# Kernel tuning notes

Measured on AMD Instinct MI355X. Metric: run time of the kernel, lower is better.

The kernel has to match this reference:

```python
import jax, jax.numpy as jnp
import numpy as np

BETA = 0.25


def setup_inputs() -> dict:
    key = jax.random.key(0)
    k1, k2 = jax.random.split(key)
    latents = jax.random.normal(k1, (16, 4096, 256), dtype=jnp.float32)
    K = 1024
    # torch init: uniform(-1/K, 1/K)
    codebook = jax.random.uniform(k2, (K, 256), dtype=jnp.float32, minval=-1.0 / K, maxval=1.0 / K)
    return {"latents": latents, "codebook": codebook}


def reference(latents, codebook):
    D = codebook.shape[1]
    flat = latents.reshape(-1, D)  # [N, D]
    dist = (jnp.sum(flat * flat, axis=1, keepdims=True)
            + jnp.sum(codebook * codebook, axis=1)
            - 2.0 * jnp.matmul(flat, codebook.T))
    encoding_inds = jnp.argmin(dist, axis=1)  # [N]
    # gather nearest codebook vectors (equivalent to one-hot @ codebook)
    quantized = codebook[encoding_inds].reshape(latents.shape)
    commitment_loss = jnp.mean((jax.lax.stop_gradient(quantized) - latents) ** 2)
    embedding_loss = jnp.mean((quantized - jax.lax.stop_gradient(latents)) ** 2)
    vq_loss = commitment_loss * BETA + embedding_loss
    # straight-through estimator
    quantized_st = latents + jax.lax.stop_gradient(quantized - latents)
    return quantized_st, vq_loss
```

## Files before the change

kernel.cpp:

```cpp
#include <hip/hip_runtime.h>

typedef __attribute__((ext_vector_type(4))) float f32x4;
typedef __attribute__((ext_vector_type(2))) long i64x2;

#define SCALE 262144.0f
#define NEG2S -524288.0f
#define INV_S2 1.4551915228366852e-11f

static __device__ __forceinline__ unsigned umin2(unsigned a, unsigned b) { return a < b ? a : b; }

static __device__ __forceinline__ float dec_e4m3(unsigned b) {
  int e = (b >> 3) & 15, m = b & 7;
  float v = e ? ldexpf((float)(8 + m), e - 10) : ldexpf((float)m, -9);
  return (b & 0x80) ? -v : v;
}

__global__ void vq_prep(const float* __restrict__ cb,
                        float* __restrict__ norms,
                        unsigned char* __restrict__ cbh,
                        float* __restrict__ loss_out) {
  if (blockIdx.x == 0 && threadIdx.x == 0) *loss_out = 0.0f;
  const int lane = threadIdx.x & 63;
  const int code = (blockIdx.x * blockDim.x + threadIdx.x) >> 6;
  const f32x4 v = ((const f32x4*)(cb + (long)code * 256))[lane];
  unsigned w = __builtin_amdgcn_cvt_pk_fp8_f32(v[0] * SCALE, v[1] * SCALE, 0, false);
  w = __builtin_amdgcn_cvt_pk_fp8_f32(v[2] * SCALE, v[3] * SCALE, w, true);
  float n = 0.f;
#pragma unroll
  for (int j = 0; j < 4; ++j) {
    float d = dec_e4m3((w >> (8 * j)) & 0xFFu);
    n = __builtin_fmaf(d, d, n);
  }
  const int newpos = ((lane >> 1) & 3) * 64 + (lane >> 3) * 8 + (lane & 1) * 4;
  *(unsigned*)(cbh + (long)code * 256 + newpos) = w;
#pragma unroll
  for (int m = 1; m < 64; m <<= 1) n += __shfl_xor(n, m);
  if (lane == 0) norms[code] = n;
}

#define BM 128
#define DD 256
#define NTHR 512
#define CT 64
#define NSUB 16

__global__ __launch_bounds__(NTHR, 4)
void vq_main(const float* __restrict__ X,
             const float* __restrict__ CB,
             const float* __restrict__ norms_g,
             const unsigned char* __restrict__ cbh,
             float* __restrict__ out,
             float* __restrict__ loss_out,
             float lscale) {
  __shared__ __attribute__((aligned(16))) unsigned char Eb[2 * CT * DD];
  __shared__ __attribute__((aligned(16))) float nrmLds[1024];
  __shared__ float wsumX[8];
  __shared__ float wsumS[8];

  const int t = threadIdx.x;
  const int lane = t & 63;
  const int wave = t >> 6;
  const int lo16 = lane & 15;
  const int hi = lane >> 4;
  const long rowBase = (long)blockIdx.x * BM;

  const char* cbB = (const char*)cbh;
  char* ebBase = (char*)Eb;
#define STAGE_E(ST, BUF)                                                                      \
  {                                                                                           \
    _Pragma("unroll") for (int c = 0; c < 2; ++c) {                                           \
      unsigned o = (unsigned)(wave * 2048 + c * 1024 + lane * 16);                            \
      unsigned src = o ^ ((((o >> 8) & 7u)) << 4);                                            \
      __builtin_amdgcn_global_load_lds(                                                       \
          (const __attribute__((address_space(1))) void*)(cbB + (unsigned)(ST)*16384u + src), \
          (__attribute__((address_space(3))) void*)(ebBase + (BUF)*16384 + wave * 2048 + c * 1024), \
          16, 0, 0);                                                                          \
    }                                                                                         \
  }

  STAGE_E(0, 0);

  nrmLds[t] = norms_g[t];
  nrmLds[t + 512] = norms_g[t + 512];

  float xn = 0.f;
  long a[8];
  {
    const f32x4* xr = (const f32x4*)(X + (rowBase + wave * 16 + lo16) * DD);
#pragma unroll
    for (int ks = 0; ks < 8; ++ks) {
      f32x4 v0 = __builtin_nontemporal_load(xr + ks * 8 + hi * 2);
      f32x4 v1 = __builtin_nontemporal_load(xr + ks * 8 + hi * 2 + 1);
#pragma unroll
      for (int j = 0; j < 4; ++j) xn = __builtin_fmaf(v0[j], v0[j], xn);
#pragma unroll
      for (int j = 0; j < 4; ++j) xn = __builtin_fmaf(v1[j], v1[j], xn);
      unsigned w0 = __builtin_amdgcn_cvt_pk_fp8_f32(v0[0], v0[1], 0, false);
      w0 = __builtin_amdgcn_cvt_pk_fp8_f32(v0[2], v0[3], w0, true);
      unsigned w1 = __builtin_amdgcn_cvt_pk_fp8_f32(v1[0], v1[1], 0, false);
      w1 = __builtin_amdgcn_cvt_pk_fp8_f32(v1[2], v1[3], w1, true);
      a[ks] = (long)w0 | ((long)w1 << 32);
    }
  }
  __syncthreads();

  unsigned best[4];
#pragma unroll
  for (int r = 0; r < 4; ++r) best[r] = 0xFFFFFFFFu;

  const unsigned swzl = (unsigned)((lo16 & 7) << 4);
  unsigned nbase[4];
#pragma unroll
  for (int n = 0; n < 4; ++n) nbase[n] = (unsigned)((n * 16 + lo16) * 256) ^ swzl;
  const unsigned hi64 = (unsigned)(hi * 64);

#pragma unroll 2
  for (int st = 0; st < NSUB; ++st) {
    if (st + 1 < NSUB) {
      STAGE_E(st + 1, (st + 1) & 1);
      asm volatile("s_waitcnt vmcnt(2)" ::: "memory");
    } else {
      asm volatile("s_waitcnt vmcnt(0)" ::: "memory");
    }
    __builtin_amdgcn_s_barrier();
    __builtin_amdgcn_sched_barrier(0);

    const char* eb = ebBase + (st & 1) * 16384;
    f32x4 acc[4];
#pragma unroll
    for (int n = 0; n < 4; ++n) {
      f32x4 z = {0.f, 0.f, 0.f, 0.f};
      acc[n] = z;
    }
    __builtin_amdgcn_s_setprio(1);
#pragma unroll
    for (int kp = 0; kp < 4; ++kp) {
      const unsigned koff = hi64 + (unsigned)(kp * 16);
      i64x2 b0 = *(const i64x2*)(eb + (nbase[0] ^ koff));
      i64x2 b1 = *(const i64x2*)(eb + (nbase[1] ^ koff));
      i64x2 b2 = *(const i64x2*)(eb + (nbase[2] ^ koff));
      i64x2 b3 = *(const i64x2*)(eb + (nbase[3] ^ koff));
      acc[0] = __builtin_amdgcn_mfma_f32_16x16x32_fp8_fp8(a[2 * kp], b0.x, acc[0], 0, 0, 0);
      acc[1] = __builtin_amdgcn_mfma_f32_16x16x32_fp8_fp8(a[2 * kp], b1.x, acc[1], 0, 0, 0);
      acc[2] = __builtin_amdgcn_mfma_f32_16x16x32_fp8_fp8(a[2 * kp], b2.x, acc[2], 0, 0, 0);
      acc[3] = __builtin_amdgcn_mfma_f32_16x16x32_fp8_fp8(a[2 * kp], b3.x, acc[3], 0, 0, 0);
      acc[0] = __builtin_amdgcn_mfma_f32_16x16x32_fp8_fp8(a[2 * kp + 1], b0.y, acc[0], 0, 0, 0);
      acc[1] = __builtin_amdgcn_mfma_f32_16x16x32_fp8_fp8(a[2 * kp + 1], b1.y, acc[1], 0, 0, 0);
      acc[2] = __builtin_amdgcn_mfma_f32_16x16x32_fp8_fp8(a[2 * kp + 1], b2.y, acc[2], 0, 0, 0);
      acc[3] = __builtin_amdgcn_mfma_f32_16x16x32_fp8_fp8(a[2 * kp + 1], b3.y, acc[3], 0, 0, 0);
    }
    __builtin_amdgcn_s_setprio(0);

#pragma unroll
    for (int n = 0; n < 4; ++n) {
      float nf = nrmLds[st * 64 + n * 16 + lo16];
      unsigned code = (unsigned)(st * 64 + n * 16 + lo16);
#pragma unroll
      for (int r = 0; r < 4; ++r) {
        float sv = __builtin_fmaf(NEG2S, acc[n][r], nf);
        unsigned u = __float_as_uint(sv);
        u = ((int)u < 0) ? ~u : (u | 0x80000000u);
        best[r] = umin2(best[r], (u & 0xFFFFFC00u) | code);
      }
    }

    __builtin_amdgcn_sched_barrier(0);
    __builtin_amdgcn_s_barrier();
  }

#pragma unroll
  for (int r = 0; r < 4; ++r) {
#pragma unroll
    for (int msk = 1; msk < 16; msk <<= 1)
      best[r] = umin2(best[r], (unsigned)__shfl_xor((int)best[r], msk));
  }

#pragma unroll
  for (int msk = 1; msk < 64; msk <<= 1) xn += __shfl_xor(xn, msk);
  if (lane == 0) wsumX[wave] = xn;

  __syncthreads();
  unsigned* mg = (unsigned*)Eb;
  unsigned* idxArr = mg + BM;
  if (lo16 == 0) {
#pragma unroll
    for (int r = 0; r < 4; ++r) {
      mg[wave * 16 + hi * 4 + r] = best[r];
    }
  }
  __syncthreads();
  float sc = 0.f;
  if (t < BM) {
    unsigned e = mg[t];
    idxArr[t] = e & 1023u;
    unsigned um = (e & 0xFFFFFC00u) | 512u;
    float sr = (um & 0x80000000u) ? __uint_as_float(um & 0x7FFFFFFFu) : __uint_as_float(~um);
    sc = sr * INV_S2;
  }
#pragma unroll
  for (int msk = 1; msk < 64; msk <<= 1) sc += __shfl_xor(sc, msk);
  if (lane == 0) wsumS[wave] = sc;
  __syncthreads();

  {
    const f32x4* CBv = (const f32x4*)CB;
    f32x4* Og = (f32x4*)(out + rowBase * DD);
#pragma unroll 4
    for (int i = 0; i < 16; ++i) {
      int idx = t + NTHR * i;
      int row = idx >> 6, d4 = idx & 63;
      int code = (int)idxArr[row];
      f32x4 e = CBv[code * 64 + d4];
      __builtin_nontemporal_store(e, Og + idx);
    }
  }

  if (t == 0) {
    float tot = 0.f;
#pragma unroll
    for (int w = 0; w < 8; ++w) tot += wsumX[w] + wsumS[w];
    atomicAdd(loss_out, tot * lscale);
  }
}

extern "C" void kernel_launch(void* const* d_in, const int* in_sizes, int n_in,
                              void* d_out, int out_size, void* d_ws, size_t ws_size,
                              hipStream_t stream) {
  const float* X = (const float*)d_in[0];
  const float* CB = (const float*)d_in[1];
  float* out = (float*)d_out;

  const int ND = in_sizes[0];
  const int K = in_sizes[1] / DD;
  const int N = ND / DD;

  float* ws_norms = (float*)d_ws;
  unsigned char* ws_cb = (unsigned char*)((char*)d_ws + 4096);
  float* loss_out = out + (size_t)ND;

  vq_prep<<<K / 4, 256, 0, stream>>>(CB, ws_norms, ws_cb, loss_out);

  const float lscale = 1.25f / (float)ND;
  vq_main<<<N / BM, NTHR, 0, stream>>>(X, CB, ws_norms, ws_cb, out, loss_out, lscale);
}
```

Before: 56.95 us.

## Keep codebook slice resident in registers and stream latent tiles through LDS

Swaps the dataflow so each wave keeps its 128-code fp8 codebook slice and norms in registers for the whole block. 16-row latent tiles are converted to fp8 and double-buffered in LDS, and each wave writes its own per-tile argmin candidates for a final cross-wave min. Blocks now cover 256 rows instead of 128, and occupancy is lowered to 2 blocks per SIMD set to hold 64 extra registers of B fragments. This removes repeated streaming of the whole codebook through LDS per block. The cost is heavier register pressure, a barrier per tile, and fewer blocks in the grid.

Result: slower. 62.70 us (+10.1%).

```diff
diff --git a/kernel.cpp b/kernel.cpp
--- a/kernel.cpp
+++ b/kernel.cpp
@@ -38,13 +38,11 @@
   if (lane == 0) norms[code] = n;
 }
 
-#define BM 128
-#define DD 256
 #define NTHR 512
-#define CT 64
-#define NSUB 16
-
-__global__ __launch_bounds__(NTHR, 4)
+#define RPB 256
+#define NTILE 16
+
+__global__ __launch_bounds__(NTHR, 2)
 void vq_main(const float* __restrict__ X,
              const float* __restrict__ CB,
              const float* __restrict__ norms_g,
@@ -52,161 +50,146 @@
              float* __restrict__ out,
              float* __restrict__ loss_out,
              float lscale) {
-  __shared__ __attribute__((aligned(16))) unsigned char Eb[2 * CT * DD];
-  __shared__ __attribute__((aligned(16))) float nrmLds[1024];
-  __shared__ float wsumX[8];
-  __shared__ float wsumS[8];
+  __shared__ __attribute__((aligned(16))) unsigned char Xs[2][4096];
+  __shared__ unsigned mgAll[NTILE][8][16];
+  __shared__ unsigned idxArr[RPB];
+  __shared__ float wsumX[8], wsumS[8];
 
   const int t = threadIdx.x;
   const int lane = t & 63;
   const int wave = t >> 6;
   const int lo16 = lane & 15;
   const int hi = lane >> 4;
-  const long rowBase = (long)blockIdx.x * BM;
-
-  const char* cbB = (const char*)cbh;
-  char* ebBase = (char*)Eb;
-#define STAGE_E(ST, BUF)                                                                      \
-  {                                                                                           \
-    _Pragma("unroll") for (int c = 0; c < 2; ++c) {                                           \
-      unsigned o = (unsigned)(wave * 2048 + c * 1024 + lane * 16);                            \
-      unsigned src = o ^ ((((o >> 8) & 7u)) << 4);                                            \
-      __builtin_amdgcn_global_load_lds(                                                       \
-          (const __attribute__((address_space(1))) void*)(cbB + (unsigned)(ST)*16384u + src), \
-          (__attribute__((address_space(3))) void*)(ebBase + (BUF)*16384 + wave * 2048 + c * 1024), \
-          16, 0, 0);                                                                          \
-    }                                                                                         \
-  }
-
-  STAGE_E(0, 0);
-
-  nrmLds[t] = norms_g[t];
-  nrmLds[t + 512] = norms_g[t + 512];
+  const long rowBase = (long)blockIdx.x * RPB;
+
+  long b[8][8];
+  float nrm[8];
+  {
+    const char* cbB = (const char*)cbh;
+#pragma unroll
+    for (int n = 0; n < 8; ++n) {
+      const int code = wave * 128 + n * 16 + lo16;
+      const char* src = cbB + (long)code * 256 + hi * 64;
+#pragma unroll
+      for (int kp = 0; kp < 4; ++kp) {
+        i64x2 bb = *(const i64x2*)(src + kp * 16);
+        b[n][2 * kp] = bb.x;
+        b[n][2 * kp + 1] = bb.y;
+      }
+      nrm[n] = norms_g[code];
+    }
+  }
+
+  const int srow = t >> 5;
+  const int sch = t & 31;
+  const unsigned sdst =
+      (unsigned)(srow * 256 + ((((sch & 3) * 64) + ((sch >> 2) * 8)) ^ ((srow & 7) << 3)));
+  const f32x4* xv = (const f32x4*)(X + (rowBase + srow) * 256) + sch * 2;
 
   float xn = 0.f;
-  long a[8];
-  {
-    const f32x4* xr = (const f32x4*)(X + (rowBase + wave * 16 + lo16) * DD);
-#pragma unroll
-    for (int ks = 0; ks < 8; ++ks) {
-      f32x4 v0 = __builtin_nontemporal_load(xr + ks * 8 + hi * 2);
-      f32x4 v1 = __builtin_nontemporal_load(xr + ks * 8 + hi * 2 + 1);
-#pragma unroll
-      for (int j = 0; j < 4; ++j) xn = __builtin_fmaf(v0[j], v0[j], xn);
-#pragma unroll
-      for (int j = 0; j < 4; ++j) xn = __builtin_fmaf(v1[j], v1[j], xn);
-      unsigned w0 = __builtin_amdgcn_cvt_pk_fp8_f32(v0[0], v0[1], 0, false);
-      w0 = __builtin_amdgcn_cvt_pk_fp8_f32(v0[2], v0[3], w0, true);
-      unsigned w1 = __builtin_amdgcn_cvt_pk_fp8_f32(v1[0], v1[1], 0, false);
-      w1 = __builtin_amdgcn_cvt_pk_fp8_f32(v1[2], v1[3], w1, true);
-      a[ks] = (long)w0 | ((long)w1 << 32);
-    }
-  }
+  f32x4 p0, p1;
+
+#define CVT_WRITE(BUF)                                                                    \
+  {                                                                                       \
+    float s0 = 0.f;                                                                       \
+    _Pragma("unroll") for (int j = 0; j < 4; ++j) s0 = __builtin_fmaf(p0[j], p0[j], s0);  \
+    _Pragma("unroll") for (int j = 0; j < 4; ++j) s0 = __builtin_fmaf(p1[j], p1[j], s0);  \
+    xn += s0;                                                                             \
+    unsigned w0 = __builtin_amdgcn_cvt_pk_fp8_f32(p0[0], p0[1], 0, false);                \
+    w0 = __builtin_amdgcn_cvt_pk_fp8_f32(p0[2], p0[3], w0, true);                         \
+    unsigned w1 = __builtin_amdgcn_cvt_pk_fp8_f32(p1[0], p1[1], 0, false);                \
+    w1 = __builtin_amdgcn_cvt_pk_fp8_f32(p1[2], p1[3], w1, true);                         \
+    *(long*)((char*)&Xs[BUF][0] + sdst) = (long)(unsigned)w0 | ((long)w1 << 32);          \
+  }
+
+  p0 = __builtin_nontemporal_load(xv);
+  p1 = __builtin_nontemporal_load(xv + 1);
+  CVT_WRITE(0);
+  p0 = __builtin_nontemporal_load(xv + 1024);
+  p1 = __builtin_nontemporal_load(xv + 1024 + 1);
   __syncthreads();
 
-  unsigned best[4];
-#pragma unroll
-  for (int r = 0; r < 4; ++r) best[r] = 0xFFFFFFFFu;
-
-  const unsigned swzl = (unsigned)((lo16 & 7) << 4);
-  unsigned nbase[4];
-#pragma unroll
-  for (int n = 0; n < 4; ++n) nbase[n] = (unsigned)((n * 16 + lo16) * 256) ^ swzl;
-  const unsigned hi64 = (unsigned)(hi * 64);
-
-#pragma unroll 2
-  for (int st = 0; st < NSUB; ++st) {
-    if (st + 1 < NSUB) {
-      STAGE_E(st + 1, (st + 1) & 1);
-      asm volatile("s_waitcnt vmcnt(2)" ::: "memory");
-    } else {
-      asm volatile("s_waitcnt vmcnt(0)" ::: "memory");
-    }
-    __builtin_amdgcn_s_barrier();
-    __builtin_amdgcn_sched_barrier(0);
-
-    const char* eb = ebBase + (st & 1) * 16384;
-    f32x4 acc[4];
-#pragma unroll
-    for (int n = 0; n < 4; ++n) {
+  for (int tt = 0; tt < NTILE; ++tt) {
+    const char* xb = (const char*)&Xs[tt & 1][0];
+    const unsigned abase = (unsigned)(lo16 * 256 + hi * 64);
+    const unsigned aswz = (unsigned)((lo16 & 7) << 3);
+    long a[8];
+#pragma unroll
+    for (int ks = 0; ks < 8; ++ks)
+      a[ks] = *(const long*)(xb + ((abase + ks * 8) ^ aswz));
+
+    f32x4 acc[8];
+#pragma unroll
+    for (int n = 0; n < 8; ++n) {
       f32x4 z = {0.f, 0.f, 0.f, 0.f};
       acc[n] = z;
     }
     __builtin_amdgcn_s_setprio(1);
 #pragma unroll
-    for (int kp = 0; kp < 4; ++kp) {
-      const unsigned koff = hi64 + (unsigned)(kp * 16);
-      i64x2 b0 = *(const i64x2*)(eb + (nbase[0] ^ koff));
-      i64x2 b1 = *(const i64x2*)(eb + (nbase[1] ^ koff));
-      i64x2 b2 = *(const i64x2*)(eb + (nbase[2] ^ koff));
-      i64x2 b3 = *(const i64x2*)(eb + (nbase[3] ^ koff));
-      acc[0] = __builtin_amdgcn_mfma_f32_16x16x32_fp8_fp8(a[2 * kp], b0.x, acc[0], 0, 0, 0);
-      acc[1] = __builtin_amdgcn_mfma_f32_16x16x32_fp8_fp8(a[2 * kp], b1.x, acc[1], 0, 0, 0);
-      acc[2] = __builtin_amdgcn_mfma_f32_16x16x32_fp8_fp8(a[2 * kp], b2.x, acc[2], 0, 0, 0);
-      acc[3] = __builtin_amdgcn_mfma_f32_16x16x32_fp8_fp8(a[2 * kp], b3.x, acc[3], 0, 0, 0);
-      acc[0] = __builtin_amdgcn_mfma_f32_16x16x32_fp8_fp8(a[2 * kp + 1], b0.y, acc[0], 0, 0, 0);
-      acc[1] = __builtin_amdgcn_mfma_f32_16x16x32_fp8_fp8(a[2 * kp + 1], b1.y, acc[1], 0, 0, 0);
-      acc[2] = __builtin_amdgcn_mfma_f32_16x16x32_fp8_fp8(a[2 * kp + 1], b2.y, acc[2], 0, 0, 0);
-      acc[3] = __builtin_amdgcn_mfma_f32_16x16x32_fp8_fp8(a[2 * kp + 1], b3.y, acc[3], 0, 0, 0);
-    }
+    for (int ks = 0; ks < 8; ++ks)
+#pragma unroll
+      for (int n = 0; n < 8; ++n)
+        acc[n] = __builtin_amdgcn_mfma_f32_16x16x32_fp8_fp8(a[ks], b[n][ks], acc[n], 0, 0, 0);
     __builtin_amdgcn_s_setprio(0);
 
-#pragma unroll
-    for (int n = 0; n < 4; ++n) {
-      float nf = nrmLds[st * 64 + n * 16 + lo16];
-      unsigned code = (unsigned)(st * 64 + n * 16 + lo16);
+    unsigned bst[4] = {0xFFFFFFFFu, 0xFFFFFFFFu, 0xFFFFFFFFu, 0xFFFFFFFFu};
+#pragma unroll
+    for (int n = 0; n < 8; ++n) {
+      const float nf = nrm[n];
+      const unsigned code = (unsigned)(wave * 128 + n * 16 + lo16);
 #pragma unroll
       for (int r = 0; r < 4; ++r) {
         float sv = __builtin_fmaf(NEG2S, acc[n][r], nf);
         unsigned u = __float_as_uint(sv);
         u = ((int)u < 0) ? ~u : (u | 0x80000000u);
-        best[r] = umin2(best[r], (u & 0xFFFFFC00u) | code);
+        bst[r] = umin2(bst[r], (u & 0xFFFFFC00u) | code);
       }
     }
-
-    __builtin_amdgcn_sched_barrier(0);
-    __builtin_amdgcn_s_barrier();
-  }
-
-#pragma unroll
-  for (int r = 0; r < 4; ++r) {
-#pragma unroll
-    for (int msk = 1; msk < 16; msk <<= 1)
-      best[r] = umin2(best[r], (unsigned)__shfl_xor((int)best[r], msk));
+#pragma unroll
+    for (int r = 0; r < 4; ++r) {
+#pragma unroll
+      for (int msk = 1; msk < 16; msk <<= 1)
+        bst[r] = umin2(bst[r], (unsigned)__shfl_xor((int)bst[r], msk));
+    }
+    if (lo16 == 0) {
+#pragma unroll
+      for (int r = 0; r < 4; ++r) mgAll[tt][wave][hi * 4 + r] = bst[r];
+    }
+
+    if (tt + 1 < NTILE) {
+      CVT_WRITE((tt + 1) & 1);
+      if (tt + 2 < NTILE) {
+        p0 = __builtin_nontemporal_load(xv + (tt + 2) * 1024);
+        p1 = __builtin_nontemporal_load(xv + (tt + 2) * 1024 + 1);
+      }
+    }
+    __syncthreads();
   }
 
 #pragma unroll
   for (int msk = 1; msk < 64; msk <<= 1) xn += __shfl_xor(xn, msk);
   if (lane == 0) wsumX[wave] = xn;
 
-  __syncthreads();
-  unsigned* mg = (unsigned*)Eb;
-  unsigned* idxArr = mg + BM;
-  if (lo16 == 0) {
-#pragma unroll
-    for (int r = 0; r < 4; ++r) {
-      mg[wave * 16 + hi * 4 + r] = best[r];
-    }
-  }
-  __syncthreads();
-  float sc = 0.f;
-  if (t < BM) {
-    unsigned e = mg[t];
+  float scv = 0.f;
+  if (t < RPB) {
+    unsigned e = 0xFFFFFFFFu;
+#pragma unroll
+    for (int w = 0; w < 8; ++w) e = umin2(e, mgAll[t >> 4][w][t & 15]);
     idxArr[t] = e & 1023u;
     unsigned um = (e & 0xFFFFFC00u) | 512u;
     float sr = (um & 0x80000000u) ? __uint_as_float(um & 0x7FFFFFFFu) : __uint_as_float(~um);
-    sc = sr * INV_S2;
-  }
-#pragma unroll
-  for (int msk = 1; msk < 64; msk <<= 1) sc += __shfl_xor(sc, msk);
-  if (lane == 0) wsumS[wave] = sc;
+    scv = sr * INV_S2;
+  }
+#pragma unroll
+  for (int msk = 1; msk < 64; msk <<= 1) scv += __shfl_xor(scv, msk);
+  if (lane == 0) wsumS[wave] = scv;
   __syncthreads();
 
   {
     const f32x4* CBv = (const f32x4*)CB;
-    f32x4* Og = (f32x4*)(out + rowBase * DD);
+    f32x4* Og = (f32x4*)(out + rowBase * 256);
 #pragma unroll 4
-    for (int i = 0; i < 16; ++i) {
+    for (int i = 0; i < 32; ++i) {
       int idx = t + NTHR * i;
       int row = idx >> 6, d4 = idx & 63;
       int code = (int)idxArr[row];
@@ -231,8 +214,8 @@
   float* out = (float*)d_out;
 
   const int ND = in_sizes[0];
-  const int K = in_sizes[1] / DD;
-  const int N = ND / DD;
+  const int K = in_sizes[1] / 256;
+  const int N = ND / 256;
 
   float* ws_norms = (float*)d_ws;
   unsigned char* ws_cb = (unsigned char*)((char*)d_ws + 4096);
@@ -241,5 +224,5 @@
   vq_prep<<<K / 4, 256, 0, stream>>>(CB, ws_norms, ws_cb, loss_out);
 
   const float lscale = 1.25f / (float)ND;
-  vq_main<<<N / BM, NTHR, 0, stream>>>(X, CB, ws_norms, ws_cb, out, loss_out, lscale);
-}
+  vq_main<<<N / RPB, NTHR, 0, stream>>>(X, CB, ws_norms, ws_cb, out, loss_out, lscale);
+}
```

## Retile waves as 4x2 grid sharing A and B fragments, merge via LDS atomicMin

Applied to the files above, without the earlier changes.

Waves are rearranged from 8 row-strips (16 rows x 64 codes each) into a 4x2 grid where each wave handles 32 rows x 32 codes. Each B fragment read from LDS now feeds two MFMAs, which halves per-wave LDS reads of the codebook tile, at the cost of doubling the A registers. The per-row argmin across the two column waves is merged with LDS atomicMin into a keys array, which removes one barrier and the staging array. The X norm is counted once per row pair by zeroing it for the wc=1 waves.

Measured after the change: 63.61 us. +11.7%, slower.

```diff
diff --git a/kernel.cpp b/kernel.cpp
--- a/kernel.cpp
+++ b/kernel.cpp
@@ -41,7 +41,6 @@
 #define BM 128
 #define DD 256
 #define NTHR 512
-#define CT 64
 #define NSUB 16
 
 __global__ __launch_bounds__(NTHR, 4)
@@ -52,14 +51,17 @@
              float* __restrict__ out,
              float* __restrict__ loss_out,
              float lscale) {
-  __shared__ __attribute__((aligned(16))) unsigned char Eb[2 * CT * DD];
+  __shared__ __attribute__((aligned(16))) unsigned char Eb[2 * 16384];
   __shared__ __attribute__((aligned(16))) float nrmLds[1024];
+  __shared__ unsigned keys[BM];
   __shared__ float wsumX[8];
   __shared__ float wsumS[8];
 
   const int t = threadIdx.x;
   const int lane = t & 63;
   const int wave = t >> 6;
+  const int wr = wave >> 1;
+  const int wc = wave & 1;
   const int lo16 = lane & 15;
   const int hi = lane >> 4;
   const long rowBase = (long)blockIdx.x * BM;
@@ -82,11 +84,13 @@
 
   nrmLds[t] = norms_g[t];
   nrmLds[t + 512] = norms_g[t + 512];
+  if (t < BM) keys[t] = 0xFFFFFFFFu;
 
   float xn = 0.f;
-  long a[8];
-  {
-    const f32x4* xr = (const f32x4*)(X + (rowBase + wave * 16 + lo16) * DD);
+  long a[2][8];
+#pragma unroll
+  for (int s = 0; s < 2; ++s) {
+    const f32x4* xr = (const f32x4*)(X + (rowBase + wr * 32 + s * 16 + lo16) * DD);
 #pragma unroll
     for (int ks = 0; ks < 8; ++ks) {
       f32x4 v0 = __builtin_nontemporal_load(xr + ks * 8 + hi * 2);
@@ -99,19 +103,21 @@
       w0 = __builtin_amdgcn_cvt_pk_fp8_f32(v0[2], v0[3], w0, true);
       unsigned w1 = __builtin_amdgcn_cvt_pk_fp8_f32(v1[0], v1[1], 0, false);
       w1 = __builtin_amdgcn_cvt_pk_fp8_f32(v1[2], v1[3], w1, true);
-      a[ks] = (long)w0 | ((long)w1 << 32);
+      a[s][ks] = (long)w0 | ((long)w1 << 32);
     }
   }
   __syncthreads();
 
-  unsigned best[4];
-#pragma unroll
-  for (int r = 0; r < 4; ++r) best[r] = 0xFFFFFFFFu;
+  unsigned best[2][4];
+#pragma unroll
+  for (int s = 0; s < 2; ++s)
+#pragma unroll
+    for (int r = 0; r < 4; ++r) best[s][r] = 0xFFFFFFFFu;
 
   const unsigned swzl = (unsigned)((lo16 & 7) << 4);
-  unsigned nbase[4];
-#pragma unroll
-  for (int n = 0; n < 4; ++n) nbase[n] = (unsigned)((n * 16 + lo16) * 256) ^ swzl;
+  unsigned nbase[2];
+#pragma unroll
+  for (int n = 0; n < 2; ++n) nbase[n] = (unsigned)((wc * 32 + n * 16 + lo16) * 256) ^ swzl;
   const unsigned hi64 = (unsigned)(hi * 64);
 
 #pragma unroll 2
@@ -126,42 +132,44 @@
     __builtin_amdgcn_sched_barrier(0);
 
     const char* eb = ebBase + (st & 1) * 16384;
-    f32x4 acc[4];
-#pragma unroll
-    for (int n = 0; n < 4; ++n) {
-      f32x4 z = {0.f, 0.f, 0.f, 0.f};
-      acc[n] = z;
-    }
+    f32x4 acc[2][2];
+#pragma unroll
+    for (int s = 0; s < 2; ++s)
+#pragma unroll
+      for (int n = 0; n < 2; ++n) {
+        f32x4 z = {0.f, 0.f, 0.f, 0.f};
+        acc[s][n] = z;
+      }
     __builtin_amdgcn_s_setprio(1);
 #pragma unroll
     for (int kp = 0; kp < 4; ++kp) {
       const unsigned koff = hi64 + (unsigned)(kp * 16);
       i64x2 b0 = *(const i64x2*)(eb + (nbase[0] ^ koff));
       i64x2 b1 = *(const i64x2*)(eb + (nbase[1] ^ koff));
-      i64x2 b2 = *(const i64x2*)(eb + (nbase[2] ^ koff));
-      i64x2 b3 = *(const i64x2*)(eb + (nbase[3] ^ koff));
-      acc[0] = __builtin_amdgcn_mfma_f32_16x16x32_fp8_fp8(a[2 * kp], b0.x, acc[0], 0, 0, 0);
-      acc[1] = __builtin_amdgcn_mfma_f32_16x16x32_fp8_fp8(a[2 * kp], b1.x, acc[1], 0, 0, 0);
-      acc[2] = __builtin_amdgcn_mfma_f32_16x16x32_fp8_fp8(a[2 * kp], b2.x, acc[2], 0, 0, 0);
-      acc[3] = __builtin_amdgcn_mfma_f32_16x16x32_fp8_fp8(a[2 * kp], b3.x, acc[3], 0, 0, 0);
-      acc[0] = __builtin_amdgcn_mfma_f32_16x16x32_fp8_fp8(a[2 * kp + 1], b0.y, acc[0], 0, 0, 0);
-      acc[1] = __builtin_amdgcn_mfma_f32_16x16x32_fp8_fp8(a[2 * kp + 1], b1.y, acc[1], 0, 0, 0);
-      acc[2] = __builtin_amdgcn_mfma_f32_16x16x32_fp8_fp8(a[2 * kp + 1], b2.y, acc[2], 0, 0, 0);
-      acc[3] = __builtin_amdgcn_mfma_f32_16x16x32_fp8_fp8(a[2 * kp + 1], b3.y, acc[3], 0, 0, 0);
+      acc[0][0] = __builtin_amdgcn_mfma_f32_16x16x32_fp8_fp8(a[0][2 * kp], b0.x, acc[0][0], 0, 0, 0);
+      acc[1][0] = __builtin_amdgcn_mfma_f32_16x16x32_fp8_fp8(a[1][2 * kp], b0.x, acc[1][0], 0, 0, 0);
+      acc[0][1] = __builtin_amdgcn_mfma_f32_16x16x32_fp8_fp8(a[0][2 * kp], b1.x, acc[0][1], 0, 0, 0);
+      acc[1][1] = __builtin_amdgcn_mfma_f32_16x16x32_fp8_fp8(a[1][2 * kp], b1.x, acc[1][1], 0, 0, 0);
+      acc[0][0] = __builtin_amdgcn_mfma_f32_16x16x32_fp8_fp8(a[0][2 * kp + 1], b0.y, acc[0][0], 0, 0, 0);
+      acc[1][0] = __builtin_amdgcn_mfma_f32_16x16x32_fp8_fp8(a[1][2 * kp + 1], b0.y, acc[1][0], 0, 0, 0);
+      acc[0][1] = __builtin_amdgcn_mfma_f32_16x16x32_fp8_fp8(a[0][2 * kp + 1], b1.y, acc[0][1], 0, 0, 0);
+      acc[1][1] = __builtin_amdgcn_mfma_f32_16x16x32_fp8_fp8(a[1][2 * kp + 1], b1.y, acc[1][1], 0, 0, 0);
     }
     __builtin_amdgcn_s_setprio(0);
 
 #pragma unroll
-    for (int n = 0; n < 4; ++n) {
-      float nf = nrmLds[st * 64 + n * 16 + lo16];
-      unsigned code = (unsigned)(st * 64 + n * 16 + lo16);
-#pragma unroll
-      for (int r = 0; r < 4; ++r) {
-        float sv = __builtin_fmaf(NEG2S, acc[n][r], nf);
-        unsigned u = __float_as_uint(sv);
-        u = ((int)u < 0) ? ~u : (u | 0x80000000u);
-        best[r] = umin2(best[r], (u & 0xFFFFFC00u) | code);
-      }
+    for (int n = 0; n < 2; ++n) {
+      float nf = nrmLds[st * 64 + wc * 32 + n * 16 + lo16];
+      unsigned code = (unsigned)(st * 64 + wc * 32 + n * 16 + lo16);
+#pragma unroll
+      for (int s = 0; s < 2; ++s)
+#pragma unroll
+        for (int r = 0; r < 4; ++r) {
+          float sv = __builtin_fmaf(NEG2S, acc[s][n][r], nf);
+          unsigned u = __float_as_uint(sv);
+          u = ((int)u < 0) ? ~u : (u | 0x80000000u);
+          best[s][r] = umin2(best[s][r], (u & 0xFFFFFC00u) | code);
+        }
     }
 
     __builtin_amdgcn_sched_barrier(0);
@@ -169,30 +177,31 @@
   }
 
 #pragma unroll
-  for (int r = 0; r < 4; ++r) {
-#pragma unroll
-    for (int msk = 1; msk < 16; msk <<= 1)
-      best[r] = umin2(best[r], (unsigned)__shfl_xor((int)best[r], msk));
+  for (int s = 0; s < 2; ++s)
+#pragma unroll
+    for (int r = 0; r < 4; ++r) {
+#pragma unroll
+      for (int msk = 1; msk < 16; msk <<= 1)
+        best[s][r] = umin2(best[s][r], (unsigned)__shfl_xor((int)best[s][r], msk));
+    }
+  if (lo16 == 0) {
+#pragma unroll
+    for (int s = 0; s < 2; ++s)
+#pragma unroll
+      for (int r = 0; r < 4; ++r) {
+        atomicMin(&keys[wr * 32 + s * 16 + hi * 4 + r], best[s][r]);
+      }
   }
 
 #pragma unroll
   for (int msk = 1; msk < 64; msk <<= 1) xn += __shfl_xor(xn, msk);
-  if (lane == 0) wsumX[wave] = xn;
+  if (lane == 0) wsumX[wave] = wc ? 0.0f : xn;
 
   __syncthreads();
-  unsigned* mg = (unsigned*)Eb;
-  unsigned* idxArr = mg + BM;
-  if (lo16 == 0) {
-#pragma unroll
-    for (int r = 0; r < 4; ++r) {
-      mg[wave * 16 + hi * 4 + r] = best[r];
-    }
-  }
-  __syncthreads();
+
   float sc = 0.f;
   if (t < BM) {
-    unsigned e = mg[t];
-    idxArr[t] = e & 1023u;
+    unsigned e = keys[t];
     unsigned um = (e & 0xFFFFFC00u) | 512u;
     float sr = (um & 0x80000000u) ? __uint_as_float(um & 0x7FFFFFFFu) : __uint_as_float(~um);
     sc = sr * INV_S2;
@@ -200,7 +209,6 @@
 #pragma unroll
   for (int msk = 1; msk < 64; msk <<= 1) sc += __shfl_xor(sc, msk);
   if (lane == 0) wsumS[wave] = sc;
-  __syncthreads();
 
   {
     const f32x4* CBv = (const f32x4*)CB;
@@ -209,12 +217,13 @@
     for (int i = 0; i < 16; ++i) {
       int idx = t + NTHR * i;
       int row = idx >> 6, d4 = idx & 63;
-      int code = (int)idxArr[row];
+      int code = (int)(keys[row] & 1023u);
       f32x4 e = CBv[code * 64 + d4];
       __builtin_nontemporal_store(e, Og + idx);
     }
   }
 
+  __syncthreads();
   if (t == 0) {
     float tot = 0.f;
 #pragma unroll
```
